# Kernel optimization log

Measured on AMD Instinct MI355X. Metric: run time of the kernel, lower is better.

Reference implementation:

```python
import jax, jax.numpy as jnp
import numpy as np

D_MODEL = 2048
K_DIM = 128
V_DIM = 128
H = 16
B = 1
S = 2048
SCALE_BASE = 512.0
THETA = 10000.0
EPS = 1e-5


def setup_inputs() -> dict:
    key = jax.random.key(0)
    ks = jax.random.split(key, 11)
    lin = lambda k, i, o: jax.random.normal(k, (i, o), jnp.float32) * 0.02
    return {
        "x": jax.random.normal(ks[0], (B, S, D_MODEL), jnp.float32),
        "Wq": lin(ks[1], D_MODEL, K_DIM * H), "bq": jnp.zeros((K_DIM * H,), jnp.float32),
        "Wk": lin(ks[2], D_MODEL, K_DIM * H), "bk": jnp.zeros((K_DIM * H,), jnp.float32),
        "Wv": lin(ks[3], D_MODEL, V_DIM * H), "bv": jnp.zeros((V_DIM * H,), jnp.float32),
        "Wg": lin(ks[4], D_MODEL, V_DIM * H), "bg": jnp.zeros((V_DIM * H,), jnp.float32),
        "Wo": lin(ks[5], V_DIM * H, D_MODEL), "bo": jnp.zeros((D_MODEL,), jnp.float32),
    }


def _rotate_half(x):
    # interleaved pairs: (x0, x1, x2, x3, ...) -> (-x1, x0, -x3, x2, ...)
    xr = x.reshape(*x.shape[:-1], -1, 2)
    x1, x2 = xr[..., 0], xr[..., 1]
    return jnp.stack((-x2, x1), axis=-1).reshape(x.shape)


def _rope_xpos(q, k, seq_len, dim):
    pos = jnp.arange(seq_len, dtype=jnp.float32)
    inv_freq = 1.0 / (THETA ** (jnp.arange(0, dim, 2, dtype=jnp.float32) / dim))
    freqs = jnp.repeat(pos[:, None] * inv_freq[None, :], 2, axis=-1)  # (S, dim)
    cos, sin = jnp.cos(freqs), jnp.sin(freqs)
    sbase = (jnp.arange(0, dim, 2, dtype=jnp.float32) + 0.4 * dim) / (1.4 * dim)
    power = (pos - seq_len // 2) / SCALE_BASE
    scale = jnp.repeat(sbase[None, :] ** power[:, None], 2, axis=-1)  # (S, dim)
    q = (q * cos + _rotate_half(q) * sin) * scale
    k = (k * cos + _rotate_half(k) * sin) / scale
    return q, k


def reference(x, Wq, bq, Wk, bk, Wv, bv, Wg, bg, Wo, bo):
    Bb, Ss, Dd = x.shape
    heads = lambda t: t.reshape(Bb, Ss, H, -1).transpose(0, 2, 1, 3)  # (B,H,S,d)
    q = heads(x @ Wq + bq)
    k = heads(x @ Wk + bk)
    v = heads(x @ Wv + bv)
    q, k = _rope_xpos(q, k, Ss, K_DIM)
    # per-head decay gamma_h = 1 - 2^{-5-h}
    gamma = 1.0 - 2.0 ** (-5.0 - jnp.arange(H, dtype=jnp.float32))
    pos = jnp.arange(Ss, dtype=jnp.float32)
    pm = pos[:, None] - pos[None, :]  # (S,S)
    decay_mask = jnp.where(pm >= 0, gamma[:, None, None] ** jnp.maximum(pm, 0.0), 0.0)  # (H,S,S)
    scores = jnp.einsum('bhid,bhjd->bhij', q, k) * decay_mask
    ret = jnp.einsum('bhij,bhjd->bhid', scores, v)  # (B,H,S,V_DIM)
    # concat heads and GroupNorm (num_groups=H, affine=False) over flattened rows
    concat = ret.transpose(0, 2, 1, 3).reshape(Bb * Ss, H, V_DIM)
    mu = concat.mean(-1, keepdims=True)
    var = ((concat - mu) ** 2).mean(-1, keepdims=True)
    gn = ((concat - mu) / jnp.sqrt(var + EPS)).reshape(Bb, Ss, H * V_DIM)
    out = (jax.nn.silu(x @ Wg + bg) * gn) @ Wo + bo
    return out
```

## Files before the change

### kernel.cpp

```cpp
#include <hip/hip_runtime.h>
#include <hip/hip_bf16.h>

#define S 2048
#define DM 2048
#define H 16
#define HD 128

using bf16 = __hip_bfloat16;
typedef __attribute__((ext_vector_type(8))) short bf16x8;
typedef __attribute__((ext_vector_type(8))) unsigned short u16x8;
typedef __attribute__((ext_vector_type(4))) float f32x4;

__device__ __forceinline__ unsigned short f2bu(float f) {
  bf16 b = __float2bfloat16(f);
  union { bf16 b; unsigned short u; } cv; cv.b = b; return cv.u;
}
__device__ __forceinline__ float bu2f(unsigned short u) {
  union { bf16 b; unsigned short u; } cv; cv.u = u; return __bfloat162float(cv.b);
}

__device__ __forceinline__ void async_copy16(const void* g, void* l) {
  __builtin_amdgcn_global_load_lds(
      (const __attribute__((address_space(1))) void*)g,
      (__attribute__((address_space(3))) void*)l, 16, 0, 0);
}

__global__ __launch_bounds__(256) void cvt_kernel(const float* __restrict__ x,
                                                  unsigned short* __restrict__ o) {
  int i = (blockIdx.x * 256 + threadIdx.x) * 4;
  float4 v = *(const float4*)(x + i);
  ushort4 r;
  r.x = f2bu(v.x); r.y = f2bu(v.y); r.z = f2bu(v.z); r.w = f2bu(v.w);
  *(ushort4*)(o + i) = r;
}

__global__ __launch_bounds__(256) void wtrans_kernel(
    const float* __restrict__ s0, const float* __restrict__ s1, const float* __restrict__ s2,
    const float* __restrict__ s3, const float* __restrict__ s4,
    unsigned short* __restrict__ d0, unsigned short* __restrict__ d1, unsigned short* __restrict__ d2,
    unsigned short* __restrict__ d3, unsigned short* __restrict__ d4) {
  __shared__ float tile[64][65];
  int z = blockIdx.z;
  const float* src = z == 0 ? s0 : z == 1 ? s1 : z == 2 ? s2 : z == 3 ? s3 : s4;
  unsigned short* dst = z == 0 ? d0 : z == 1 ? d1 : z == 2 ? d2 : z == 3 ? d3 : d4;
  int tid = threadIdx.x;
  int by = blockIdx.y * 64;
  int bx = blockIdx.x * 64;
  int r0 = tid >> 4;
  int c0 = (tid & 15) * 4;
#pragma unroll
  for (int i = 0; i < 4; i++) {
    int row = r0 + i * 16;
    float4 t = *(const float4*)(src + (size_t)(by + row) * DM + bx + c0);
    tile[row][c0 + 0] = t.x; tile[row][c0 + 1] = t.y;
    tile[row][c0 + 2] = t.z; tile[row][c0 + 3] = t.w;
  }
  __syncthreads();
#pragma unroll
  for (int i = 0; i < 4; i++) {
    int nrow = r0 + i * 16;
    ushort4 o;
    o.x = f2bu(tile[c0 + 0][nrow]);
    o.y = f2bu(tile[c0 + 1][nrow]);
    o.z = f2bu(tile[c0 + 2][nrow]);
    o.w = f2bu(tile[c0 + 3][nrow]);
    *(ushort4*)(dst + (size_t)(bx + nrow) * DM + by + c0) = o;
  }
}

__global__ __launch_bounds__(256) void vtrans_kernel(const unsigned short* __restrict__ v,
                                                     unsigned short* __restrict__ vt) {
  __shared__ unsigned short tile[64][72];
  int tid = threadIdx.x;
  int by = blockIdx.y * 64, bx = blockIdx.x * 64;
  int r0 = tid >> 3;
  int c0 = (tid & 7) * 8;
#pragma unroll
  for (int i = 0; i < 2; i++) {
    int row = r0 + i * 32;
    u16x8 t = *(const u16x8*)(v + (size_t)(by + row) * DM + bx + c0);
#pragma unroll
    for (int j = 0; j < 8; j++) tile[row][c0 + j] = t[j];
  }
  __syncthreads();
#pragma unroll
  for (int i = 0; i < 2; i++) {
    int nrow = r0 + i * 32;
    u16x8 o;
#pragma unroll
    for (int j = 0; j < 8; j++) o[j] = tile[c0 + j][nrow];
    *(u16x8*)(vt + (size_t)(bx + nrow) * DM + by + c0) = o;
  }
}

__device__ __forceinline__ void stage_half(const unsigned short* gbase, char* ldsbase, int tid) {
#pragma unroll
  for (int r = 0; r < 2; r++) {
    int a = r * 8192 + tid * 16;
    int row = a >> 7;
    int cb = (a & 127) ^ ((row & 7) << 4);
    async_copy16((const unsigned char*)(gbase + (size_t)row * DM) + cb, ldsbase + a);
  }
}

__global__ __launch_bounds__(512, 2) void gemm_qkvg_kernel(
    const unsigned short* __restrict__ A, const unsigned short* __restrict__ Bm,
    const float* __restrict__ bias0, const float* __restrict__ bias1,
    const float* __restrict__ bias2, const float* __restrict__ bias3,
    unsigned short* __restrict__ C0, unsigned short* __restrict__ C1,
    unsigned short* __restrict__ C2, unsigned short* __restrict__ C3) {
  __shared__ alignas(16) char smem[131072];
  char* sA = smem;
  char* sB = smem + 65536;
  int tid = threadIdx.x;
  int wg = blockIdx.y * 32 + blockIdx.x;
  int swz = (wg & 7) * 32 + (wg >> 3);
  int bm = (swz >> 5) * 256;
  int bn = (swz & 31) * 256;
  int wid = tid >> 6, lane = tid & 63;
  int wm = wid >> 2, wn = wid & 3;
  int r16 = lane & 15, quad = lane >> 4;
  f32x4 acc[8][4] = {};
  bf16x8 bfrag[2][4];
  const int bhalf = (wn >> 1) << 14;
  const int blr0 = ((wn & 1) << 6) + r16;

  stage_half(Bm + (size_t)bn * DM, sB, tid);
  stage_half(Bm + (size_t)(bn + 128) * DM, sB + 16384, tid);
  stage_half(A + (size_t)bm * DM, sA, tid);
  stage_half(A + (size_t)(bm + 128) * DM, sA + 16384, tid);
  asm volatile("s_waitcnt vmcnt(0)" ::: "memory");
  __builtin_amdgcn_s_barrier();

  for (int t = 0; t < 32; ++t) {
    const int buf = (t & 1) << 15;
    const int nbuf = buf ^ 32768;
    const bool more = t < 31;
    const int kn = (t + 1) * 64;
    char* sAc = sA + buf;
    char* sBc = sB + buf;
    bf16x8 afrag[4];

#pragma unroll
    for (int nt = 0; nt < 4; ++nt) {
      int lr = blr0 + nt * 16;
      bfrag[0][nt] = *(const bf16x8*)(sBc + bhalf + lr * 128 + ((quad * 16) ^ ((lr & 7) << 4)));
    }
#pragma unroll
    for (int mt = 0; mt < 4; ++mt) {
      int lr = mt * 32 + wm * 16 + r16;
      afrag[mt] = *(const bf16x8*)(sAc + lr * 128 + ((quad * 16) ^ ((lr & 7) << 4)));
    }
    if (more) stage_half(Bm + (size_t)bn * DM + kn, sB + nbuf, tid);
    __builtin_amdgcn_s_barrier();
    asm volatile("s_waitcnt lgkmcnt(0)" ::: "memory");
    __builtin_amdgcn_s_setprio(1);
#pragma unroll
    for (int mt = 0; mt < 4; ++mt)
#pragma unroll
      for (int nt = 0; nt < 4; ++nt)
        acc[mt][nt] = __builtin_amdgcn_mfma_f32_16x16x32_bf16(afrag[mt], bfrag[0][nt], acc[mt][nt], 0, 0, 0);
    __builtin_amdgcn_s_setprio(0);
    __builtin_amdgcn_s_barrier();

#pragma unroll
    for (int nt = 0; nt < 4; ++nt) {
      int lr = blr0 + nt * 16;
      bfrag[1][nt] = *(const bf16x8*)(sBc + bhalf + lr * 128 + ((64 + quad * 16) ^ ((lr & 7) << 4)));
    }
#pragma unroll
    for (int mt = 0; mt < 4; ++mt) {
      int lr = mt * 32 + wm * 16 + r16;
      afrag[mt] = *(const bf16x8*)(sAc + lr * 128 + ((64 + quad * 16) ^ ((lr & 7) << 4)));
    }
    if (more) stage_half(Bm + (size_t)(bn + 128) * DM + kn, sB + nbuf + 16384, tid);
    __builtin_amdgcn_s_barrier();
    asm volatile("s_waitcnt lgkmcnt(0)" ::: "memory");
    __builtin_amdgcn_s_setprio(1);
#pragma unroll
    for (int mt = 0; mt < 4; ++mt)
#pragma unroll
      for (int nt = 0; nt < 4; ++nt)
        acc[mt][nt] = __builtin_amdgcn_mfma_f32_16x16x32_bf16(afrag[mt], bfrag[1][nt], acc[mt][nt], 0, 0, 0);
    __builtin_amdgcn_s_setprio(0);
    if (more) { asm volatile("s_waitcnt vmcnt(4)" ::: "memory"); }
    else      { asm volatile("s_waitcnt vmcnt(0)" ::: "memory"); }
    __builtin_amdgcn_s_barrier();

#pragma unroll
    for (int mt = 0; mt < 4; ++mt) {
      int lr = mt * 32 + wm * 16 + r16;
      afrag[mt] = *(const bf16x8*)(sAc + 16384 + lr * 128 + ((quad * 16) ^ ((lr & 7) << 4)));
    }
    if (more) stage_half(A + (size_t)bm * DM + kn, sA + nbuf, tid);
    __builtin_amdgcn_s_barrier();
    asm volatile("s_waitcnt lgkmcnt(0)" ::: "memory");
    __builtin_amdgcn_s_setprio(1);
#pragma unroll
    for (int mt = 0; mt < 4; ++mt)
#pragma unroll
      for (int nt = 0; nt < 4; ++nt)
        acc[4 + mt][nt] = __builtin_amdgcn_mfma_f32_16x16x32_bf16(afrag[mt], bfrag[0][nt], acc[4 + mt][nt], 0, 0, 0);
    __builtin_amdgcn_s_setprio(0);
    __builtin_amdgcn_s_barrier();

#pragma unroll
    for (int mt = 0; mt < 4; ++mt) {
      int lr = mt * 32 + wm * 16 + r16;
      afrag[mt] = *(const bf16x8*)(sAc + 16384 + lr * 128 + ((64 + quad * 16) ^ ((lr & 7) << 4)));
    }
    if (more) stage_half(A + (size_t)(bm + 128) * DM + kn, sA + nbuf + 16384, tid);
    __builtin_amdgcn_s_barrier();
    asm volatile("s_waitcnt lgkmcnt(0)" ::: "memory");
    __builtin_amdgcn_s_setprio(1);
#pragma unroll
    for (int mt = 0; mt < 4; ++mt)
#pragma unroll
      for (int nt = 0; nt < 4; ++nt)
        acc[4 + mt][nt] = __builtin_amdgcn_mfma_f32_16x16x32_bf16(afrag[mt], bfrag[1][nt], acc[4 + mt][nt], 0, 0, 0);
    __builtin_amdgcn_s_setprio(0);
    if (more) { asm volatile("s_waitcnt vmcnt(2)" ::: "memory"); }
    __builtin_amdgcn_s_barrier();
  }

  int ch = bn >> 11;
  const float* bp = ch == 0 ? bias0 : ch == 1 ? bias1 : ch == 2 ? bias2 : bias3;
  unsigned short* Cp = ch == 0 ? C0 : ch == 1 ? C1 : ch == 2 ? C2 : C3;
  int lcb = bn & 2047;
#pragma unroll
  for (int nt = 0; nt < 4; ++nt) {
    int lc = lcb + wn * 64 + nt * 16 + r16;
    float bv = bp[lc];
#pragma unroll
    for (int mt = 0; mt < 8; ++mt) {
      int m0 = bm + (mt >> 2) * 128 + (mt & 3) * 32 + wm * 16 + quad * 4;
#pragma unroll
      for (int rr = 0; rr < 4; ++rr)
        Cp[(size_t)(m0 + rr) * DM + lc] = f2bu(acc[mt][nt][rr] + bv);
    }
  }
}

__global__ __launch_bounds__(256) void gemm_out_kernel(
    const unsigned short* __restrict__ A, const unsigned short* __restrict__ Bp,
    const float* __restrict__ bias, float* __restrict__ C) {
  __shared__ alignas(16) unsigned char sA[16384];
  __shared__ alignas(16) unsigned char sB[16384];
  int tid = threadIdx.x;
  int bm = blockIdx.y * 128, bn = blockIdx.x * 128;
  int wid = tid >> 6, lane = tid & 63;
  int wm = wid >> 1, wn = wid & 1;
  int r16 = lane & 15, quad = lane >> 4;
  f32x4 acc[4][4] = {};
  for (int kt = 0; kt < DM; kt += 64) {
#pragma unroll
    for (int r = 0; r < 4; r++) {
      int a = r * 4096 + tid * 16;
      int row = a >> 7;
      int cb = (a & 127) ^ ((row & 7) << 4);
      async_copy16((const unsigned char*)(A + (size_t)(bm + row) * DM + kt) + cb, sA + a);
      async_copy16((const unsigned char*)(Bp + (size_t)(bn + row) * DM + kt) + cb, sB + a);
    }
    __syncthreads();
#pragma unroll
    for (int kk = 0; kk < 2; kk++) {
      bf16x8 af[4], bfr[4];
#pragma unroll
      for (int mt = 0; mt < 4; mt++) {
        int row = wm * 64 + mt * 16 + r16;
        af[mt] = *(const bf16x8*)(sA + row * 128 + ((quad * 16 + kk * 64) ^ ((row & 7) << 4)));
      }
#pragma unroll
      for (int nt = 0; nt < 4; nt++) {
        int row = wn * 64 + nt * 16 + r16;
        bfr[nt] = *(const bf16x8*)(sB + row * 128 + ((quad * 16 + kk * 64) ^ ((row & 7) << 4)));
      }
#pragma unroll
      for (int mt = 0; mt < 4; mt++)
#pragma unroll
        for (int nt = 0; nt < 4; nt++)
          acc[mt][nt] = __builtin_amdgcn_mfma_f32_16x16x32_bf16(af[mt], bfr[nt], acc[mt][nt], 0, 0, 0);
    }
    __syncthreads();
  }
#pragma unroll
  for (int nt = 0; nt < 4; nt++) {
    int n = bn + wn * 64 + nt * 16 + r16;
    float bv = bias[n];
#pragma unroll
    for (int mt = 0; mt < 4; mt++) {
      int m0 = bm + wm * 64 + mt * 16 + quad * 4;
#pragma unroll
      for (int r = 0; r < 4; r++)
        C[(size_t)(m0 + r) * DM + n] = acc[mt][nt][r] + bv;
    }
  }
}

__global__ __launch_bounds__(256) void rope_kernel(unsigned short* __restrict__ q,
                                                   unsigned short* __restrict__ k) {
  int idx = blockIdx.x * 256 + threadIdx.x;
  int s = idx >> 10;
  int p = idx & 1023;
  int t = p & 63;
  int head = p >> 6;
  int col = (head << 7) + (t << 1);
  size_t off = (size_t)s * DM + col;
  float ang = (float)s * exp2f((float)(-2 * t) * (13.287712379549449f / 128.0f));
  float sn, cs;
  sincosf(ang, &sn, &cs);
  float sb = ((float)(2 * t) + 51.2f) * (1.0f / 179.2f);
  float power = ((float)s - 1024.0f) * (1.0f / 512.0f);
  float scale = exp2f(power * log2f(sb));
  float l2g = log2f(1.0f - exp2f((float)(-5 - head)));
  float qsc = scale * exp2f((float)s * l2g);
  float ksc = (1.0f / scale) * exp2f(-(float)s * l2g);
  unsigned int qu = *(unsigned int*)(q + off);
  float a = bu2f(qu & 0xffff), b = bu2f(qu >> 16);
  float qa = (a * cs - b * sn) * qsc;
  float qb2 = (b * cs + a * sn) * qsc;
  *(unsigned int*)(q + off) = (unsigned int)f2bu(qa) | ((unsigned int)f2bu(qb2) << 16);
  unsigned int ku = *(unsigned int*)(k + off);
  float c2 = bu2f(ku & 0xffff), d2 = bu2f(ku >> 16);
  float ka = (c2 * cs - d2 * sn) * ksc;
  float kb2 = (d2 * cs + c2 * sn) * ksc;
  *(unsigned int*)(k + off) = (unsigned int)f2bu(ka) | ((unsigned int)f2bu(kb2) << 16);
}

__global__ __launch_bounds__(256) void retention_kernel(
    const unsigned short* __restrict__ q, const unsigned short* __restrict__ k,
    const unsigned short* __restrict__ vt, float* __restrict__ ret) {
  __shared__ alignas(16) unsigned char sK[16384];
  __shared__ alignas(16) unsigned char sV[16384];
  __shared__ alignas(16) unsigned char Plds[8192];
  int bx = blockIdx.x;
  int hi = bx >> 8;
  int h = ((bx >> 5) & 7) | (hi << 3);
  int ib = hi ? (bx & 31) : (31 - (bx & 31));
  int I = ib << 6;
  int tid = threadIdx.x, wid = tid >> 6, lane = tid & 63;
  int r16 = lane & 15, quad = lane >> 4;
  bf16x8 aQ[4];
  size_t qrow = (size_t)(I + wid * 16 + r16);
#pragma unroll
  for (int kk = 0; kk < 4; kk++)
    aQ[kk] = *(const bf16x8*)(q + qrow * DM + h * HD + kk * 32 + quad * 8);
  f32x4 acc[8] = {};
  unsigned char* Pw = Plds + wid * 2048;
  for (int J0 = 0; J0 <= I; J0 += 64) {
#pragma unroll
    for (int r = 0; r < 4; r++) {
      int a = r * 4096 + tid * 16;
      int rowk = a >> 8;
      int cbk = (a & 255) ^ ((rowk & 7) << 4);
      async_copy16((const unsigned char*)(k + (size_t)(J0 + rowk) * DM + h * HD) + cbk, sK + a);
      int rowv = a >> 7;
      int cbv = (a & 127) ^ ((rowv & 7) << 4);
      async_copy16((const unsigned char*)(vt + (size_t)(h * HD + rowv) * DM + J0) + cbv, sV + a);
    }
    __syncthreads();
    f32x4 sf[4] = {};
#pragma unroll
    for (int nt = 0; nt < 4; nt++) {
      int row = nt * 16 + r16;
#pragma unroll
      for (int kk = 0; kk < 4; kk++) {
        bf16x8 bK = *(const bf16x8*)(sK + row * 256 + ((kk * 64 + quad * 16) ^ ((row & 7) << 4)));
        sf[nt] = __builtin_amdgcn_mfma_f32_16x16x32_bf16(aQ[kk], bK, sf[nt], 0, 0, 0);
      }
    }
    bool diag = (J0 == I);
#pragma unroll
    for (int nt = 0; nt < 4; nt++) {
      int j = nt * 16 + r16;
#pragma unroll
      for (int r = 0; r < 4; r++) {
        int ii = wid * 16 + quad * 4 + r;
        float pv = sf[nt][r];
        if (diag && (ii - j) < 0) pv = 0.0f;
        int pr = quad * 4 + r;
        int pcb = (nt * 16 + r16) * 2;
        *(unsigned short*)(Pw + pr * 128 + (pcb ^ ((pr & 7) << 4))) = f2bu(pv);
      }
    }
#pragma unroll
    for (int kk2 = 0; kk2 < 2; kk2++) {
      int cb = kk2 * 64 + quad * 16;
      bf16x8 aP = *(const bf16x8*)(Pw + r16 * 128 + (cb ^ ((r16 & 7) << 4)));
#pragma unroll
      for (int nt2 = 0; nt2 < 8; nt2++) {
        int row = nt2 * 16 + r16;
        bf16x8 bV = *(const bf16x8*)(sV + row * 128 + ((kk2 * 64 + quad * 16) ^ ((row & 7) << 4)));
        acc[nt2] = __builtin_amdgcn_mfma_f32_16x16x32_bf16(aP, bV, acc[nt2], 0, 0, 0);
      }
    }
    __syncthreads();
  }
#pragma unroll
  for (int nt2 = 0; nt2 < 8; nt2++) {
    int dcol = h * HD + nt2 * 16 + r16;
#pragma unroll
    for (int r = 0; r < 4; r++) {
      int i = I + wid * 16 + quad * 4 + r;
      ret[(size_t)i * DM + dcol] = acc[nt2][r];
    }
  }
}

__global__ __launch_bounds__(256) void gn_gate_kernel(const float* __restrict__ ret,
                                                      const unsigned short* __restrict__ g,
                                                      unsigned short* __restrict__ y) {
  int tid = threadIdx.x;
  int wave = tid >> 6, lane = tid & 63;
  int gidx = blockIdx.x * 4 + wave;
  int s = gidx >> 4, h = gidx & 15;
  size_t base = (size_t)s * DM + h * HD + lane * 2;
  float2 v = *(const float2*)(ret + base);
  float sum = v.x + v.y;
  float sq = v.x * v.x + v.y * v.y;
#pragma unroll
  for (int o = 32; o > 0; o >>= 1) {
    sum += __shfl_xor(sum, o, 64);
    sq += __shfl_xor(sq, o, 64);
  }
  float mean = sum * 0.0078125f;
  float var = sq * 0.0078125f - mean * mean;
  float rstd = rsqrtf(var + 1e-5f);
  unsigned int gu = *(const unsigned int*)(g + base);
  float g0 = bu2f(gu & 0xffff), g1 = bu2f(gu >> 16);
  float s0 = g0 / (1.0f + expf(-g0));
  float s1 = g1 / (1.0f + expf(-g1));
  float y0 = s0 * (v.x - mean) * rstd;
  float y1 = s1 * (v.y - mean) * rstd;
  *(unsigned int*)(y + base) = (unsigned int)f2bu(y0) | ((unsigned int)f2bu(y1) << 16);
}

extern "C" void kernel_launch(void* const* d_in, const int* in_sizes, int n_in,
                              void* d_out, int out_size, void* d_ws, size_t ws_size,
                              hipStream_t stream) {
  (void)in_sizes; (void)n_in; (void)out_size; (void)ws_size;
  const float* x  = (const float*)d_in[0];
  const float* Wq = (const float*)d_in[1];
  const float* bq = (const float*)d_in[2];
  const float* Wk = (const float*)d_in[3];
  const float* bk = (const float*)d_in[4];
  const float* Wv = (const float*)d_in[5];
  const float* bv = (const float*)d_in[6];
  const float* Wg = (const float*)d_in[7];
  const float* bg = (const float*)d_in[8];
  const float* Wo = (const float*)d_in[9];
  const float* bo = (const float*)d_in[10];

  char* ws = (char*)d_ws;
  const size_t MB = 1ull << 20;
  unsigned short* xb   = (unsigned short*)(ws + 0 * MB);
  unsigned short* wcat = (unsigned short*)(ws + 8 * MB);
  unsigned short* wto  = (unsigned short*)(ws + 40 * MB);
  unsigned short* qb   = (unsigned short*)(ws + 48 * MB);
  unsigned short* kb   = (unsigned short*)(ws + 56 * MB);
  unsigned short* vb   = (unsigned short*)(ws + 64 * MB);
  unsigned short* gb   = (unsigned short*)(ws + 72 * MB);
  unsigned short* vt   = (unsigned short*)(ws + 80 * MB);
  float*          rt   = (float*)(ws + 88 * MB);
  unsigned short* yb   = (unsigned short*)(ws + 104 * MB);

  cvt_kernel<<<4096, 256, 0, stream>>>(x, xb);
  wtrans_kernel<<<dim3(32, 32, 5), 256, 0, stream>>>(
      Wq, Wk, Wv, Wg, Wo,
      wcat, wcat + (size_t)2048 * DM, wcat + (size_t)4096 * DM, wcat + (size_t)6144 * DM, wto);
  gemm_qkvg_kernel<<<dim3(32, 8), 512, 0, stream>>>(
      xb, wcat, bq, bk, bv, bg, qb, kb, vb, gb);
  rope_kernel<<<8192, 256, 0, stream>>>(qb, kb);
  vtrans_kernel<<<dim3(32, 32), 256, 0, stream>>>(vb, vt);
  retention_kernel<<<512, 256, 0, stream>>>(qb, kb, vt, rt);
  gn_gate_kernel<<<8192, 256, 0, stream>>>(rt, gb, yb);
  gemm_out_kernel<<<dim3(16, 16), 256, 0, stream>>>(yb, wto, bo, (float*)d_out);
}
```

Before: 202.9 us.

## Double-buffer K/V in retention, front-load GEMM prefetch, remap XCD tiles

```diff
diff --git a/kernel.cpp b/kernel.cpp
--- a/kernel.cpp
+++ b/kernel.cpp
@@ -114,9 +114,9 @@
   char* sB = smem + 65536;
   int tid = threadIdx.x;
   int wg = blockIdx.y * 32 + blockIdx.x;
-  int swz = (wg & 7) * 32 + (wg >> 3);
-  int bm = (swz >> 5) * 256;
-  int bn = (swz & 31) * 256;
+  int xcd = wg & 7, rr0 = wg >> 3;
+  int bm = (rr0 >> 2) * 256;
+  int bn = (xcd * 4 + (rr0 & 3)) * 256;
   int wid = tid >> 6, lane = tid & 63;
   int wm = wid >> 2, wn = wid & 3;
   int r16 = lane & 15, quad = lane >> 4;
@@ -151,7 +151,11 @@
       int lr = mt * 32 + wm * 16 + r16;
       afrag[mt] = *(const bf16x8*)(sAc + lr * 128 + ((quad * 16) ^ ((lr & 7) << 4)));
     }
-    if (more) stage_half(Bm + (size_t)bn * DM + kn, sB + nbuf, tid);
+    if (more) {
+      stage_half(Bm + (size_t)bn * DM + kn, sB + nbuf, tid);
+      stage_half(Bm + (size_t)(bn + 128) * DM + kn, sB + nbuf + 16384, tid);
+      stage_half(A + (size_t)bm * DM + kn, sA + nbuf, tid);
+    }
     __builtin_amdgcn_s_barrier();
     asm volatile("s_waitcnt lgkmcnt(0)" ::: "memory");
     __builtin_amdgcn_s_setprio(1);
@@ -173,7 +177,6 @@
       int lr = mt * 32 + wm * 16 + r16;
       afrag[mt] = *(const bf16x8*)(sAc + lr * 128 + ((64 + quad * 16) ^ ((lr & 7) << 4)));
     }
-    if (more) stage_half(Bm + (size_t)(bn + 128) * DM + kn, sB + nbuf + 16384, tid);
     __builtin_amdgcn_s_barrier();
     asm volatile("s_waitcnt lgkmcnt(0)" ::: "memory");
     __builtin_amdgcn_s_setprio(1);
@@ -183,7 +186,7 @@
       for (int nt = 0; nt < 4; ++nt)
         acc[mt][nt] = __builtin_amdgcn_mfma_f32_16x16x32_bf16(afrag[mt], bfrag[1][nt], acc[mt][nt], 0, 0, 0);
     __builtin_amdgcn_s_setprio(0);
-    if (more) { asm volatile("s_waitcnt vmcnt(4)" ::: "memory"); }
+    if (more) { asm volatile("s_waitcnt vmcnt(6)" ::: "memory"); }
     else      { asm volatile("s_waitcnt vmcnt(0)" ::: "memory"); }
     __builtin_amdgcn_s_barrier();
 
@@ -192,7 +195,7 @@
       int lr = mt * 32 + wm * 16 + r16;
       afrag[mt] = *(const bf16x8*)(sAc + 16384 + lr * 128 + ((quad * 16) ^ ((lr & 7) << 4)));
     }
-    if (more) stage_half(A + (size_t)bm * DM + kn, sA + nbuf, tid);
+    if (more) stage_half(A + (size_t)(bm + 128) * DM + kn, sA + nbuf + 16384, tid);
     __builtin_amdgcn_s_barrier();
     asm volatile("s_waitcnt lgkmcnt(0)" ::: "memory");
     __builtin_amdgcn_s_setprio(1);
@@ -209,7 +212,6 @@
       int lr = mt * 32 + wm * 16 + r16;
       afrag[mt] = *(const bf16x8*)(sAc + 16384 + lr * 128 + ((64 + quad * 16) ^ ((lr & 7) << 4)));
     }
-    if (more) stage_half(A + (size_t)(bm + 128) * DM + kn, sA + nbuf + 16384, tid);
     __builtin_amdgcn_s_barrier();
     asm volatile("s_waitcnt lgkmcnt(0)" ::: "memory");
     __builtin_amdgcn_s_setprio(1);
@@ -235,8 +237,8 @@
     for (int mt = 0; mt < 8; ++mt) {
       int m0 = bm + (mt >> 2) * 128 + (mt & 3) * 32 + wm * 16 + quad * 4;
 #pragma unroll
-      for (int rr = 0; rr < 4; ++rr)
-        Cp[(size_t)(m0 + rr) * DM + lc] = f2bu(acc[mt][nt][rr] + bv);
+      for (int rrr = 0; rrr < 4; ++rrr)
+        Cp[(size_t)(m0 + rrr) * DM + lc] = f2bu(acc[mt][nt][rrr] + bv);
     }
   }
 }
@@ -327,11 +329,27 @@
   *(unsigned int*)(k + off) = (unsigned int)f2bu(ka) | ((unsigned int)f2bu(kb2) << 16);
 }
 
+__device__ __forceinline__ void stage_kv(const unsigned short* __restrict__ k,
+                                         const unsigned short* __restrict__ vt,
+                                         int h, int J0, unsigned char* dK,
+                                         unsigned char* dV, int tid) {
+#pragma unroll
+  for (int r = 0; r < 4; r++) {
+    int a = r * 4096 + tid * 16;
+    int rowk = a >> 8;
+    int cbk = (a & 255) ^ ((rowk & 7) << 4);
+    async_copy16((const unsigned char*)(k + (size_t)(J0 + rowk) * DM + h * HD) + cbk, dK + a);
+    int rowv = a >> 7;
+    int cbv = (a & 127) ^ ((rowv & 7) << 4);
+    async_copy16((const unsigned char*)(vt + (size_t)(h * HD + rowv) * DM + J0) + cbv, dV + a);
+  }
+}
+
 __global__ __launch_bounds__(256) void retention_kernel(
     const unsigned short* __restrict__ q, const unsigned short* __restrict__ k,
     const unsigned short* __restrict__ vt, float* __restrict__ ret) {
-  __shared__ alignas(16) unsigned char sK[16384];
-  __shared__ alignas(16) unsigned char sV[16384];
+  __shared__ alignas(16) unsigned char sK[2][16384];
+  __shared__ alignas(16) unsigned char sV[2][16384];
   __shared__ alignas(16) unsigned char Plds[8192];
   int bx = blockIdx.x;
   int hi = bx >> 8;
@@ -347,25 +365,23 @@
     aQ[kk] = *(const bf16x8*)(q + qrow * DM + h * HD + kk * 32 + quad * 8);
   f32x4 acc[8] = {};
   unsigned char* Pw = Plds + wid * 2048;
+  stage_kv(k, vt, h, 0, sK[0], sV[0], tid);
   for (int J0 = 0; J0 <= I; J0 += 64) {
-#pragma unroll
-    for (int r = 0; r < 4; r++) {
-      int a = r * 4096 + tid * 16;
-      int rowk = a >> 8;
-      int cbk = (a & 255) ^ ((rowk & 7) << 4);
-      async_copy16((const unsigned char*)(k + (size_t)(J0 + rowk) * DM + h * HD) + cbk, sK + a);
-      int rowv = a >> 7;
-      int cbv = (a & 127) ^ ((rowv & 7) << 4);
-      async_copy16((const unsigned char*)(vt + (size_t)(h * HD + rowv) * DM + J0) + cbv, sV + a);
-    }
-    __syncthreads();
+    int cur = (J0 >> 6) & 1;
+    bool more = (J0 + 64) <= I;
+    if (more) stage_kv(k, vt, h, J0 + 64, sK[cur ^ 1], sV[cur ^ 1], tid);
+    if (more) { asm volatile("s_waitcnt vmcnt(8)" ::: "memory"); }
+    else      { asm volatile("s_waitcnt vmcnt(0)" ::: "memory"); }
+    __builtin_amdgcn_s_barrier();
+    const unsigned char* sKc = sK[cur];
+    const unsigned char* sVc = sV[cur];
     f32x4 sf[4] = {};
 #pragma unroll
     for (int nt = 0; nt < 4; nt++) {
       int row = nt * 16 + r16;
 #pragma unroll
       for (int kk = 0; kk < 4; kk++) {
-        bf16x8 bK = *(const bf16x8*)(sK + row * 256 + ((kk * 64 + quad * 16) ^ ((row & 7) << 4)));
+        bf16x8 bK = *(const bf16x8*)(sKc + row * 256 + ((kk * 64 + quad * 16) ^ ((row & 7) << 4)));
         sf[nt] = __builtin_amdgcn_mfma_f32_16x16x32_bf16(aQ[kk], bK, sf[nt], 0, 0, 0);
       }
     }
@@ -390,11 +406,11 @@
 #pragma unroll
       for (int nt2 = 0; nt2 < 8; nt2++) {
         int row = nt2 * 16 + r16;
-        bf16x8 bV = *(const bf16x8*)(sV + row * 128 + ((kk2 * 64 + quad * 16) ^ ((row & 7) << 4)));
+        bf16x8 bV = *(const bf16x8*)(sVc + row * 128 + ((kk2 * 64 + quad * 16) ^ ((row & 7) << 4)));
         acc[nt2] = __builtin_amdgcn_mfma_f32_16x16x32_bf16(aP, bV, acc[nt2], 0, 0, 0);
       }
     }
-    __syncthreads();
+    __builtin_amdgcn_s_barrier();
   }
 #pragma unroll
   for (int nt2 = 0; nt2 < 8; nt2++) {
```

Result: faster. 191.6 us (-5.6%).
